# Performance work log

Measured on AMD Instinct MI355X. Metric: run time of the kernel, lower is better.

## Reference

```python
import jax, jax.numpy as jnp
import numpy as np

BN_EPS = 1e-3  # Keras BatchNormalization default epsilon


def setup_inputs() -> dict:
    key = jax.random.key(0)
    ks = jax.random.split(key, 10)
    B, H, W, F, K = 16, 64, 64, 512, 32
    support = 1.0 / np.sqrt(K * F)
    fc_support = np.sqrt(1.0 / F)
    return {
        "inputs": jax.random.normal(ks[0], (B, H, W, F), dtype=jnp.float32),
        # Encoder params
        "codewords": jax.random.uniform(ks[1], (K, F), minval=-support, maxval=support, dtype=jnp.float32),
        "smoothing": jax.random.uniform(ks[2], (K,), minval=-1.0, maxval=0.0, dtype=jnp.float32),
        # BatchNorm (inference mode: moving stats) over feature axis of (B, K, F)
        "bn_gamma": jnp.ones((F,), dtype=jnp.float32),
        "bn_beta": jnp.zeros((F,), dtype=jnp.float32),
        "bn_mean": jnp.zeros((F,), dtype=jnp.float32),
        "bn_var": jnp.ones((F,), dtype=jnp.float32),
        # Dense layers
        "fc_enc_w": jax.random.uniform(ks[3], (F, F), minval=-fc_support, maxval=fc_support, dtype=jnp.float32),
        "fc_enc_b": jax.random.uniform(ks[4], (F,), minval=-fc_support, maxval=fc_support, dtype=jnp.float32),
        "fc_se_w": jax.random.uniform(ks[5], (F, 1), minval=-fc_support, maxval=fc_support, dtype=jnp.float32),
        "fc_se_b": jax.random.uniform(ks[6], (1,), minval=-fc_support, maxval=fc_support, dtype=jnp.float32),
    }


def _encoder(x, codewords, smoothing, bn_gamma, bn_beta, bn_mean, bn_var):
    # x: (B, H, W, F) -> feats (B, N, F)
    B, H, W, F = x.shape
    feats = x.reshape(B, H * W, F)
    # Squared residual norms without materializing (B, N, K, F):
    x2 = jnp.sum(feats * feats, axis=-1, keepdims=True)          # (B, N, 1)
    c2 = jnp.sum(codewords * codewords, axis=-1)                 # (K,)
    xc = jnp.einsum("bnf,kf->bnk", feats, codewords)             # (B, N, K)
    sqnorms = x2 - 2.0 * xc + c2                                 # (B, N, K)
    s = jax.nn.softmax(sqnorms * smoothing, axis=-1)             # (B, N, K)
    # sum_n s[b,n,k] * (x[b,n] - c[k]) = s^T x - c * sum_n s
    s_sum = jnp.sum(s, axis=1)                                   # (B, K)
    enc = jnp.einsum("bnk,bnf->bkf", s, feats) - s_sum[:, :, None] * codewords  # (B, K, F)
    # BatchNorm (inference) + ReLU, then aggregate over codewords
    enc_bn = (enc - bn_mean) * jax.lax.rsqrt(bn_var + BN_EPS) * bn_gamma + bn_beta
    return jnp.sum(jax.nn.relu(enc_bn), axis=1)                  # (B, F)


def reference(inputs, codewords, smoothing, bn_gamma, bn_beta, bn_mean, bn_var,
              fc_enc_w, fc_enc_b, fc_se_w, fc_se_b):
    enc = _encoder(inputs, codewords, smoothing, bn_gamma, bn_beta, bn_mean, bn_var)
    attn = jax.nn.sigmoid(enc @ fc_enc_w + fc_enc_b)             # (B, F)
    featuremaps_out = attn[:, None, None, :] * inputs            # (B, H, W, F)
    se_loss_out = enc @ fc_se_w + fc_se_b                        # (B, 1)
    return (featuremaps_out, se_loss_out)
```

## Files before the change

### kernel.cpp

```cpp
#include <hip/hip_runtime.h>
#include <hip/hip_bf16.h>
#include <math.h>

#define Bb   16
#define HWn  4096
#define Ff   512
#define Kk   32

typedef __attribute__((ext_vector_type(8))) short  short8;
typedef __attribute__((ext_vector_type(4))) float  f32x4;

#define WS_SSUM  0
#define WS_EOUT  512
#define WS_ATTN  (WS_EOUT + Bb * Ff)
#define WS_CWB   (WS_ATTN + Bb * Ff)
#define WS_C2    (WS_CWB + 8192)
#define WS_SM    (WS_C2 + 32)

#define SCR_PART 0
#define SCR_RED  16777216

__global__ void prep(const float* __restrict__ cw, const float* __restrict__ smth,
                     unsigned short* __restrict__ cwb,
                     float* __restrict__ c2l2, float* __restrict__ sml2)
{
    const int t = threadIdx.x;
    const float4* c4 = (const float4*)cw;
    #pragma unroll
    for (int j = 0; j < 16; ++j) {
        const int i = t + j * 256;
        const float4 v = c4[i];
        union { __hip_bfloat162 h; unsigned int u; } p0, p1;
        p0.h = __float22bfloat162_rn(make_float2(v.x, v.y));
        p1.h = __float22bfloat162_rn(make_float2(v.z, v.w));
        *reinterpret_cast<uint2*>(&cwb[i * 4]) = make_uint2(p0.u, p1.u);
    }
    const int k = t >> 3, sk = t & 7;
    float p = 0.f;
    #pragma unroll
    for (int j = 0; j < 16; ++j) {
        const float4 v = c4[k * 128 + sk + j * 8];
        p = fmaf(v.x, v.x, fmaf(v.y, v.y, fmaf(v.z, v.z, fmaf(v.w, v.w, p))));
    }
    p += __shfl_xor(p, 1); p += __shfl_xor(p, 2); p += __shfl_xor(p, 4);
    if (sk == 0) {
        const float L2E = 1.4426950408889634f;
        const float sm = smth[k];
        sml2[k] = sm * L2E;
        c2l2[k] = p * sm * L2E;
    }
}

__global__ __launch_bounds__(256, 2) void enc_pass(
    const float* __restrict__ x, const unsigned short* __restrict__ cwb,
    const float* __restrict__ c2l2, const float* __restrict__ sml2,
    float* __restrict__ part, float* __restrict__ s_sum)
{
    __shared__ __align__(16) unsigned short fb16[32 * 512];
    __shared__ float sN[32][36];
    __shared__ float x2s[32];
    __shared__ float sm_s[32], c2_s[32];

    const int tid  = threadIdx.x;
    const int wave = tid >> 6, lane = tid & 63;
    const int b    = blockIdx.y;
    const int cx   = blockIdx.x;
    const int row0 = cx * 128;

    if (tid < 32) { sm_s[tid] = sml2[tid]; c2_s[tid] = c2l2[tid]; }

    float acc[8][8];
    #pragma unroll
    for (int j = 0; j < 8; ++j)
        #pragma unroll
        for (int i = 0; i < 8; ++i) acc[j][i] = 0.f;
    float ssl[8] = {0.f, 0.f, 0.f, 0.f, 0.f, 0.f, 0.f, 0.f};

    for (int t = 0; t < 4; ++t) {
        if (t) __syncthreads();
        const float4* xr4 = (const float4*)(x + ((size_t)b * HWn + row0 + t * 32) * Ff);
        {
            const int n = tid >> 3, f8 = tid & 7;
            float p = 0.f;
            #pragma unroll
            for (int j = 0; j < 16; ++j) {
                const int f4 = f8 + j * 8;
                const float4 v = xr4[n * 128 + f4];
                p = fmaf(v.x, v.x, fmaf(v.y, v.y, fmaf(v.z, v.z, fmaf(v.w, v.w, p))));
                union { __hip_bfloat162 h; unsigned int u; } p0, p1;
                p0.h = __float22bfloat162_rn(make_float2(v.x, v.y));
                p1.h = __float22bfloat162_rn(make_float2(v.z, v.w));
                const int chunk = f4 >> 1;
                const int idx = n * 512 + (((chunk ^ (n & 7)) << 3) | ((f4 & 1) << 2));
                *reinterpret_cast<uint2*>(&fb16[idx]) = make_uint2(p0.u, p1.u);
            }
            p += __shfl_xor(p, 1); p += __shfl_xor(p, 2); p += __shfl_xor(p, 4);
            if (f8 == 0) x2s[n] = p;
        }
        __syncthreads();
        if (wave < 2) {
            const int col = lane & 15, g = lane >> 4;
            const int nl  = wave * 16 + col;
            f32x4 c0 = {0.f, 0.f, 0.f, 0.f}, c1 = {0.f, 0.f, 0.f, 0.f};
            const unsigned short* arow0 = cwb + col * 512 + g * 8;
            const unsigned short* arow1 = arow0 + 16 * 512;
            const int nswz = (nl & 7) << 3;
            #pragma unroll
            for (int fs = 0; fs < 16; ++fs) {
                const short8 a0 = *(const short8*)(arow0 + fs * 32);
                const short8 a1 = *(const short8*)(arow1 + fs * 32);
                const short8 bf = *(const short8*)&fb16[nl * 512 + ((((fs * 4 + g) << 3)) ^ nswz)];
                c0 = __builtin_amdgcn_mfma_f32_16x16x32_bf16(a0, bf, c0, 0, 0, 0);
                c1 = __builtin_amdgcn_mfma_f32_16x16x32_bf16(a1, bf, c1, 0, 0, 0);
            }
            const float x2v = x2s[nl];
            float lg[8];
            #pragma unroll
            for (int r = 0; r < 4; ++r) {
                const int k0 = g * 4 + r;
                lg[r]     = fmaf(sm_s[k0],      fmaf(-2.f, c0[r], x2v), c2_s[k0]);
                lg[4 + r] = fmaf(sm_s[k0 + 16], fmaf(-2.f, c1[r], x2v), c2_s[k0 + 16]);
            }
            float m = lg[0];
            #pragma unroll
            for (int j = 1; j < 8; ++j) m = fmaxf(m, lg[j]);
            m = fmaxf(m, __shfl_xor(m, 16)); m = fmaxf(m, __shfl_xor(m, 32));
            float e[8], sum = 0.f;
            #pragma unroll
            for (int j = 0; j < 8; ++j) { e[j] = exp2f(lg[j] - m); sum += e[j]; }
            sum += __shfl_xor(sum, 16); sum += __shfl_xor(sum, 32);
            const float inv = 1.f / sum;
            #pragma unroll
            for (int r = 0; r < 4; ++r) {
                const float s0 = e[r] * inv, s1 = e[4 + r] * inv;
                sN[nl][g * 4 + r]      = s0;
                sN[nl][16 + g * 4 + r] = s1;
                ssl[r] += s0; ssl[4 + r] += s1;
            }
        }
        __syncthreads();
        {
            const int kw = wave * 8;
            #pragma unroll 2
            for (int n = 0; n < 32; ++n) {
                const f32x4 s0 = *(const f32x4*)&sN[n][kw];
                const f32x4 s1 = *(const f32x4*)&sN[n][kw + 4];
                const uint4 u = *(const uint4*)&fb16[n * 512 + (((lane ^ (n & 7))) << 3)];
                float fx[8];
                fx[0] = __uint_as_float(u.x << 16);
                fx[1] = __uint_as_float(u.x & 0xffff0000u);
                fx[2] = __uint_as_float(u.y << 16);
                fx[3] = __uint_as_float(u.y & 0xffff0000u);
                fx[4] = __uint_as_float(u.z << 16);
                fx[5] = __uint_as_float(u.z & 0xffff0000u);
                fx[6] = __uint_as_float(u.w << 16);
                fx[7] = __uint_as_float(u.w & 0xffff0000u);
                #pragma unroll
                for (int j = 0; j < 4; ++j) {
                    const float sj0 = s0[j], sj1 = s1[j];
                    #pragma unroll
                    for (int i = 0; i < 8; ++i) {
                        acc[j][i]     = fmaf(sj0, fx[i], acc[j][i]);
                        acc[4 + j][i] = fmaf(sj1, fx[i], acc[4 + j][i]);
                    }
                }
            }
        }
    }
    if (wave < 2) {
        const int g = lane >> 4;
        #pragma unroll
        for (int j = 0; j < 8; ++j) {
            float v = ssl[j];
            v += __shfl_xor(v, 1); v += __shfl_xor(v, 2);
            v += __shfl_xor(v, 4); v += __shfl_xor(v, 8);
            if ((lane & 15) == 0) {
                const int k = ((j & 4) << 2) + g * 4 + (j & 3);
                atomicAdd(&s_sum[b * Kk + k], v);
            }
        }
    }
    {
        float* basep = part + (((size_t)(b * 32 + cx) * Kk) + wave * 8) * Ff + lane * 8;
        #pragma unroll
        for (int j = 0; j < 8; ++j) {
            *reinterpret_cast<float4*>(basep + j * Ff) =
                make_float4(acc[j][0], acc[j][1], acc[j][2], acc[j][3]);
            *reinterpret_cast<float4*>(basep + j * Ff + 4) =
                make_float4(acc[j][4], acc[j][5], acc[j][6], acc[j][7]);
        }
    }
}

__global__ void enc_red(const float* __restrict__ scr, float* __restrict__ outp)
{
    const int idx = blockIdx.x * 256 + threadIdx.x;
    const int b   = idx >> 14;
    const int rem = idx & 16383;
    const float* p = scr + (size_t)b * 32 * 16384 + rem;
    float a = 0.f;
    #pragma unroll
    for (int c = 0; c < 32; ++c) a += p[c * 16384];
    outp[idx] = a;
}

__global__ void enc_finish(const float* __restrict__ enc_acc,
                           const float* __restrict__ s_sum,
                           const float* __restrict__ cw,
                           const float* __restrict__ gamma,
                           const float* __restrict__ beta,
                           const float* __restrict__ mean,
                           const float* __restrict__ var,
                           const float* __restrict__ se_w,
                           const float* __restrict__ se_b,
                           float* __restrict__ enc_out,
                           float* __restrict__ se_out)
{
    __shared__ float ss[Kk];
    __shared__ float red[8];
    const int b = blockIdx.x, f = threadIdx.x;
    if (f < Kk) ss[f] = s_sum[b * Kk + f];
    __syncthreads();
    const float m  = mean[f];
    const float g  = gamma[f];
    const float bt = beta[f];
    const float iv = rsqrtf(var[f] + 1e-3f);
    float a = 0.f;
    #pragma unroll 4
    for (int k = 0; k < Kk; ++k) {
        float v = enc_acc[((long)b * Kk + k) * Ff + f] - ss[k] * cw[k * Ff + f];
        v = (v - m) * iv * g + bt;
        a += fmaxf(v, 0.f);
    }
    enc_out[b * Ff + f] = a;
    float p = a * se_w[f];
    p += __shfl_down(p, 32); p += __shfl_down(p, 16); p += __shfl_down(p, 8);
    p += __shfl_down(p, 4);  p += __shfl_down(p, 2);  p += __shfl_down(p, 1);
    if ((f & 63) == 0) red[f >> 6] = p;
    __syncthreads();
    if (f == 0) {
        float t = 0.f;
        #pragma unroll
        for (int i = 0; i < 8; ++i) t += red[i];
        se_out[b] = t + se_b[0];
    }
}

__global__ void attn_fc(const float* __restrict__ enc_out,
                        const float* __restrict__ W,
                        const float* __restrict__ bias,
                        float* __restrict__ attn)
{
    __shared__ float eo[Bb][Ff];
    const int t = threadIdx.x, fg = blockIdx.x;
    #pragma unroll
    for (int j = 0; j < 4; ++j)
        reinterpret_cast<float4*>(&eo[0][0])[t + j * 512] =
            reinterpret_cast<const float4*>(enc_out)[t + j * 512];
    __syncthreads();
    const int f  = fg * 64 + (t & 63);
    const int b0 = t >> 6;
    float a0 = bias[f], a1 = bias[f];
    #pragma unroll 8
    for (int fp = 0; fp < Ff; ++fp) {
        const float w = W[fp * Ff + f];
        a0 = fmaf(eo[b0][fp],     w, a0);
        a1 = fmaf(eo[b0 + 8][fp], w, a1);
    }
    attn[b0 * Ff + f]       = 1.f / (1.f + expf(-a0));
    attn[(b0 + 8) * Ff + f] = 1.f / (1.f + expf(-a1));
}

__global__ void bcast_mul(const float4* __restrict__ x4,
                          const float* __restrict__ attn,
                          float4* __restrict__ o4)
{
    const int stride = gridDim.x * blockDim.x;
    const int total4 = Bb * HWn * Ff / 4;
    for (int i = blockIdx.x * blockDim.x + threadIdx.x; i < total4; i += stride) {
        const float4 v = x4[i];
        const int f4 = i & 127;
        const int bb = i >> 19;
        const float4 a = *reinterpret_cast<const float4*>(&attn[bb * Ff + f4 * 4]);
        o4[i] = make_float4(v.x * a.x, v.y * a.y, v.z * a.z, v.w * a.w);
    }
}

extern "C" void kernel_launch(void* const* d_in, const int* in_sizes, int n_in,
                              void* d_out, int out_size, void* d_ws, size_t ws_size,
                              hipStream_t stream)
{
    (void)in_sizes; (void)n_in; (void)out_size; (void)ws_size;
    const float* x     = (const float*)d_in[0];
    const float* cw    = (const float*)d_in[1];
    const float* smth  = (const float*)d_in[2];
    const float* gamma = (const float*)d_in[3];
    const float* beta  = (const float*)d_in[4];
    const float* mean  = (const float*)d_in[5];
    const float* var   = (const float*)d_in[6];
    const float* Wenc  = (const float*)d_in[7];
    const float* benc  = (const float*)d_in[8];
    const float* Wse   = (const float*)d_in[9];
    const float* bse   = (const float*)d_in[10];

    float* out = (float*)d_out;
    float* ws  = (float*)d_ws;
    float* ssum = ws + WS_SSUM;
    float* eout = ws + WS_EOUT;
    float* attn = ws + WS_ATTN;
    unsigned short* cwb = (unsigned short*)(ws + WS_CWB);
    float* c2l2 = ws + WS_C2;
    float* sml2 = ws + WS_SM;

    float* scr_part = out + SCR_PART;
    float* scr_red  = out + SCR_RED;

    hipMemsetAsync(ssum, 0, (size_t)Bb * Kk * sizeof(float), stream);
    prep<<<1, 256, 0, stream>>>(cw, smth, cwb, c2l2, sml2);
    enc_pass<<<dim3(32, Bb), 256, 0, stream>>>(x, cwb, c2l2, sml2, scr_part, ssum);
    enc_red<<<1024, 256, 0, stream>>>(scr_part, scr_red);
    enc_finish<<<Bb, 512, 0, stream>>>(scr_red, ssum, cw, gamma, beta, mean, var,
                                       Wse, bse, eout, out + (long)Bb * HWn * Ff);
    attn_fc<<<8, 512, 0, stream>>>(eout, Wenc, benc, attn);
    bcast_mul<<<2048, 256, 0, stream>>>((const float4*)x, attn, (float4*)out);
}
```

Measured before the change: 172.2 us.

## Compute s^T x accumulation with bf16 MFMA and prefetch next input tile

Replaces the scalar FMA loop that accumulated softmax weights times features with bf16 MFMA instructions. This needs a transposed bf16 copy of the input tile and bf16 softmax weights in shared memory. Global loads for the next 32-row tile are issued into registers before the current tile is processed, to overlap memory latency. Rounding the softmax weights to bf16 loses some precision, and the extra transposed writes to LDS add shared-memory traffic and register pressure.

```diff
diff --git a/kernel.cpp b/kernel.cpp
--- a/kernel.cpp
+++ b/kernel.cpp
@@ -20,6 +20,17 @@
 #define SCR_PART 0
 #define SCR_RED  16777216
 
+static __device__ __forceinline__ unsigned int pack2bf(float a, float b) {
+    union { __hip_bfloat162 h; unsigned int u; } p;
+    p.h = __float22bfloat162_rn(make_float2(a, b));
+    return p.u;
+}
+static __device__ __forceinline__ unsigned short f2bf(float v) {
+    union { __hip_bfloat16 h; unsigned short u; } c;
+    c.h = __float2bfloat16(v);
+    return c.u;
+}
+
 __global__ void prep(const float* __restrict__ cw, const float* __restrict__ smth,
                      unsigned short* __restrict__ cwb,
                      float* __restrict__ c2l2, float* __restrict__ sml2)
@@ -30,10 +41,8 @@
     for (int j = 0; j < 16; ++j) {
         const int i = t + j * 256;
         const float4 v = c4[i];
-        union { __hip_bfloat162 h; unsigned int u; } p0, p1;
-        p0.h = __float22bfloat162_rn(make_float2(v.x, v.y));
-        p1.h = __float22bfloat162_rn(make_float2(v.z, v.w));
-        *reinterpret_cast<uint2*>(&cwb[i * 4]) = make_uint2(p0.u, p1.u);
+        *reinterpret_cast<uint2*>(&cwb[i * 4]) =
+            make_uint2(pack2bf(v.x, v.y), pack2bf(v.z, v.w));
     }
     const int k = t >> 3, sk = t & 7;
     float p = 0.f;
@@ -57,50 +66,77 @@
     float* __restrict__ part, float* __restrict__ s_sum)
 {
     __shared__ __align__(16) unsigned short fb16[32 * 512];
-    __shared__ float sN[32][36];
+    __shared__ __align__(16) unsigned short xTl[512 * 36];
+    __shared__ __align__(16) unsigned short sTl[32 * 32];
     __shared__ float x2s[32];
     __shared__ float sm_s[32], c2_s[32];
 
     const int tid  = threadIdx.x;
     const int wave = tid >> 6, lane = tid & 63;
+    const int col  = lane & 15, g = lane >> 4;
     const int b    = blockIdx.y;
     const int cx   = blockIdx.x;
     const int row0 = cx * 128;
 
     if (tid < 32) { sm_s[tid] = sml2[tid]; c2_s[tid] = c2l2[tid]; }
 
-    float acc[8][8];
-    #pragma unroll
-    for (int j = 0; j < 8; ++j)
-        #pragma unroll
-        for (int i = 0; i < 8; ++i) acc[j][i] = 0.f;
+    const int n2  = tid >> 4;
+    const int f16 = tid & 15;
+
+    f32x4 accm[16];
+    #pragma unroll
+    for (int i = 0; i < 16; ++i) accm[i] = (f32x4){0.f, 0.f, 0.f, 0.f};
     float ssl[8] = {0.f, 0.f, 0.f, 0.f, 0.f, 0.f, 0.f, 0.f};
+
+    const float4* xb4 = (const float4*)(x + ((size_t)b * HWn + row0) * Ff);
+    float4 r0[8], r1[8];
+    #pragma unroll
+    for (int j = 0; j < 8; ++j) {
+        r0[j] = xb4[(2 * n2) * 128 + f16 + j * 16];
+        r1[j] = xb4[(2 * n2 + 1) * 128 + f16 + j * 16];
+    }
 
     for (int t = 0; t < 4; ++t) {
         if (t) __syncthreads();
-        const float4* xr4 = (const float4*)(x + ((size_t)b * HWn + row0 + t * 32) * Ff);
         {
-            const int n = tid >> 3, f8 = tid & 7;
-            float p = 0.f;
-            #pragma unroll
-            for (int j = 0; j < 16; ++j) {
-                const int f4 = f8 + j * 8;
-                const float4 v = xr4[n * 128 + f4];
-                p = fmaf(v.x, v.x, fmaf(v.y, v.y, fmaf(v.z, v.z, fmaf(v.w, v.w, p))));
-                union { __hip_bfloat162 h; unsigned int u; } p0, p1;
-                p0.h = __float22bfloat162_rn(make_float2(v.x, v.y));
-                p1.h = __float22bfloat162_rn(make_float2(v.z, v.w));
-                const int chunk = f4 >> 1;
-                const int idx = n * 512 + (((chunk ^ (n & 7)) << 3) | ((f4 & 1) << 2));
-                *reinterpret_cast<uint2*>(&fb16[idx]) = make_uint2(p0.u, p1.u);
-            }
-            p += __shfl_xor(p, 1); p += __shfl_xor(p, 2); p += __shfl_xor(p, 4);
-            if (f8 == 0) x2s[n] = p;
+            float p0 = 0.f, p1 = 0.f;
+            const int na = 2 * n2, nb = na + 1;
+            #pragma unroll
+            for (int j = 0; j < 8; ++j) {
+                const float4 va = r0[j], vb = r1[j];
+                p0 = fmaf(va.x, va.x, fmaf(va.y, va.y, fmaf(va.z, va.z, fmaf(va.w, va.w, p0))));
+                p1 = fmaf(vb.x, vb.x, fmaf(vb.y, vb.y, fmaf(vb.z, vb.z, fmaf(vb.w, vb.w, p1))));
+                const int f4n = f16 + j * 16;
+                const int lowbit = (f4n & 1) << 2;
+                const int chA = (((f4n >> 1) ^ (na & 7)) << 3) | lowbit;
+                const int chB = (((f4n >> 1) ^ (nb & 7)) << 3) | lowbit;
+                *reinterpret_cast<uint2*>(&fb16[na * 512 + chA]) =
+                    make_uint2(pack2bf(va.x, va.y), pack2bf(va.z, va.w));
+                *reinterpret_cast<uint2*>(&fb16[nb * 512 + chB]) =
+                    make_uint2(pack2bf(vb.x, vb.y), pack2bf(vb.z, vb.w));
+                const int fbase = f4n * 4;
+                unsigned int* xw = reinterpret_cast<unsigned int*>(&xTl[0]);
+                xw[(fbase + 0) * 18 + n2] = pack2bf(va.x, vb.x);
+                xw[(fbase + 1) * 18 + n2] = pack2bf(va.y, vb.y);
+                xw[(fbase + 2) * 18 + n2] = pack2bf(va.z, vb.z);
+                xw[(fbase + 3) * 18 + n2] = pack2bf(va.w, vb.w);
+            }
+            p0 += __shfl_xor(p0, 1); p0 += __shfl_xor(p0, 2);
+            p0 += __shfl_xor(p0, 4); p0 += __shfl_xor(p0, 8);
+            p1 += __shfl_xor(p1, 1); p1 += __shfl_xor(p1, 2);
+            p1 += __shfl_xor(p1, 4); p1 += __shfl_xor(p1, 8);
+            if (f16 == 0) { x2s[na] = p0; x2s[nb] = p1; }
+        }
+        if (t < 3) {
+            #pragma unroll
+            for (int j = 0; j < 8; ++j) {
+                r0[j] = xb4[((t + 1) * 32 + 2 * n2) * 128 + f16 + j * 16];
+                r1[j] = xb4[((t + 1) * 32 + 2 * n2 + 1) * 128 + f16 + j * 16];
+            }
         }
         __syncthreads();
         if (wave < 2) {
-            const int col = lane & 15, g = lane >> 4;
-            const int nl  = wave * 16 + col;
+            const int nl = wave * 16 + col;
             f32x4 c0 = {0.f, 0.f, 0.f, 0.f}, c1 = {0.f, 0.f, 0.f, 0.f};
             const unsigned short* arow0 = cwb + col * 512 + g * 8;
             const unsigned short* arow1 = arow0 + 16 * 512;
@@ -133,42 +169,27 @@
             #pragma unroll
             for (int r = 0; r < 4; ++r) {
                 const float s0 = e[r] * inv, s1 = e[4 + r] * inv;
-                sN[nl][g * 4 + r]      = s0;
-                sN[nl][16 + g * 4 + r] = s1;
+                sTl[(g * 4 + r) * 32 + nl]        = f2bf(s0);
+                sTl[(16 + g * 4 + r) * 32 + nl]   = f2bf(s1);
                 ssl[r] += s0; ssl[4 + r] += s1;
             }
         }
         __syncthreads();
         {
-            const int kw = wave * 8;
-            #pragma unroll 2
-            for (int n = 0; n < 32; ++n) {
-                const f32x4 s0 = *(const f32x4*)&sN[n][kw];
-                const f32x4 s1 = *(const f32x4*)&sN[n][kw + 4];
-                const uint4 u = *(const uint4*)&fb16[n * 512 + (((lane ^ (n & 7))) << 3)];
-                float fx[8];
-                fx[0] = __uint_as_float(u.x << 16);
-                fx[1] = __uint_as_float(u.x & 0xffff0000u);
-                fx[2] = __uint_as_float(u.y << 16);
-                fx[3] = __uint_as_float(u.y & 0xffff0000u);
-                fx[4] = __uint_as_float(u.z << 16);
-                fx[5] = __uint_as_float(u.z & 0xffff0000u);
-                fx[6] = __uint_as_float(u.w << 16);
-                fx[7] = __uint_as_float(u.w & 0xffff0000u);
-                #pragma unroll
-                for (int j = 0; j < 4; ++j) {
-                    const float sj0 = s0[j], sj1 = s1[j];
-                    #pragma unroll
-                    for (int i = 0; i < 8; ++i) {
-                        acc[j][i]     = fmaf(sj0, fx[i], acc[j][i]);
-                        acc[4 + j][i] = fmaf(sj1, fx[i], acc[4 + j][i]);
-                    }
-                }
+            const int koff = (wave & 1) << 4;
+            const int fh   = (wave >> 1) << 8;
+            const short8 afrag = *(const short8*)&sTl[(koff + col) * 32 + g * 8];
+            #pragma unroll
+            for (int fb = 0; fb < 16; ++fb) {
+                const unsigned short* bp = &xTl[(fh + fb * 16 + col) * 36 + g * 8];
+                union { uint2 u[2]; short8 s; } bu;
+                bu.u[0] = *reinterpret_cast<const uint2*>(bp);
+                bu.u[1] = *reinterpret_cast<const uint2*>(bp + 4);
+                accm[fb] = __builtin_amdgcn_mfma_f32_16x16x32_bf16(afrag, bu.s, accm[fb], 0, 0, 0);
             }
         }
     }
     if (wave < 2) {
-        const int g = lane >> 4;
         #pragma unroll
         for (int j = 0; j < 8; ++j) {
             float v = ssl[j];
@@ -181,14 +202,14 @@
         }
     }
     {
-        float* basep = part + (((size_t)(b * 32 + cx) * Kk) + wave * 8) * Ff + lane * 8;
+        const int koff = (wave & 1) << 4;
+        const int fh   = (wave >> 1) << 8;
+        float* basep = part + ((size_t)(b * 32 + cx) * Kk + koff + g * 4) * Ff + fh + col;
         #pragma unroll
-        for (int j = 0; j < 8; ++j) {
-            *reinterpret_cast<float4*>(basep + j * Ff) =
-                make_float4(acc[j][0], acc[j][1], acc[j][2], acc[j][3]);
-            *reinterpret_cast<float4*>(basep + j * Ff + 4) =
-                make_float4(acc[j][4], acc[j][5], acc[j][6], acc[j][7]);
-        }
+        for (int fb = 0; fb < 16; ++fb)
+            #pragma unroll
+            for (int r = 0; r < 4; ++r)
+                basep[r * Ff + fb * 16] = accm[fb][r];
     }
 }
 
```

Result: faster. 157.6 us (-8.5%).

## Use 512-thread blocks with 64-row tiles and split MFMA/softmax across all waves

Applied to the files above, without the earlier changes.

The encoder pass moves from 256 to 512 threads per block and stages 64 rows per tile instead of 32, so each block runs two tile iterations instead of four. All eight waves now take part in the MFMA distance computation, each computing one 16x16 tile, and the softmax is spread across all threads through a shared scratch transpose. Previously only two waves did that work while the rest sat idle. Each wave's accumulator drops to 4x8, which lowers register pressure, and the s_sum reduction goes through shared memory so only 32 atomics are issued per block. The cost is extra __syncthreads barriers and more LDS use per block, which may limit occupancy.

```diff
diff --git a/kernel.cpp b/kernel.cpp
--- a/kernel.cpp
+++ b/kernel.cpp
@@ -6,6 +6,8 @@
 #define HWn  4096
 #define Ff   512
 #define Kk   32
+#define ROWS 64
+#define GCH  32
 
 typedef __attribute__((ext_vector_type(8))) short  short8;
 typedef __attribute__((ext_vector_type(4))) float  f32x4;
@@ -20,6 +22,12 @@
 #define SCR_PART 0
 #define SCR_RED  16777216
 
+static __device__ __forceinline__ unsigned int pack2bf(float a, float b) {
+    union { __hip_bfloat162 h; unsigned int u; } p;
+    p.h = __float22bfloat162_rn(make_float2(a, b));
+    return p.u;
+}
+
 __global__ void prep(const float* __restrict__ cw, const float* __restrict__ smth,
                      unsigned short* __restrict__ cwb,
                      float* __restrict__ c2l2, float* __restrict__ sml2)
@@ -30,10 +38,8 @@
     for (int j = 0; j < 16; ++j) {
         const int i = t + j * 256;
         const float4 v = c4[i];
-        union { __hip_bfloat162 h; unsigned int u; } p0, p1;
-        p0.h = __float22bfloat162_rn(make_float2(v.x, v.y));
-        p1.h = __float22bfloat162_rn(make_float2(v.z, v.w));
-        *reinterpret_cast<uint2*>(&cwb[i * 4]) = make_uint2(p0.u, p1.u);
+        *reinterpret_cast<uint2*>(&cwb[i * 4]) =
+            make_uint2(pack2bf(v.x, v.y), pack2bf(v.z, v.w));
     }
     const int k = t >> 3, sk = t & 7;
     float p = 0.f;
@@ -51,101 +57,106 @@
     }
 }
 
-__global__ __launch_bounds__(256, 2) void enc_pass(
+__global__ __launch_bounds__(512, 4) void enc_pass(
     const float* __restrict__ x, const unsigned short* __restrict__ cwb,
     const float* __restrict__ c2l2, const float* __restrict__ sml2,
     float* __restrict__ part, float* __restrict__ s_sum)
 {
-    __shared__ __align__(16) unsigned short fb16[32 * 512];
-    __shared__ float sN[32][36];
-    __shared__ float x2s[32];
+    __shared__ __align__(16) unsigned short fb16[ROWS * 512];
+    __shared__ float scratch[2304];
+    __shared__ float x2s[ROWS];
     __shared__ float sm_s[32], c2_s[32];
+    __shared__ float swred[8][32];
 
     const int tid  = threadIdx.x;
     const int wave = tid >> 6, lane = tid & 63;
+    const int col  = lane & 15, g = lane >> 4;
     const int b    = blockIdx.y;
     const int cx   = blockIdx.x;
-    const int row0 = cx * 128;
 
     if (tid < 32) { sm_s[tid] = sml2[tid]; c2_s[tid] = c2l2[tid]; }
 
-    float acc[8][8];
-    #pragma unroll
-    for (int j = 0; j < 8; ++j)
+    const int srow = tid >> 3;
+    const int sf   = tid & 7;
+
+    float acc[4][8];
+    #pragma unroll
+    for (int j = 0; j < 4; ++j)
         #pragma unroll
         for (int i = 0; i < 8; ++i) acc[j][i] = 0.f;
-    float ssl[8] = {0.f, 0.f, 0.f, 0.f, 0.f, 0.f, 0.f, 0.f};
-
-    for (int t = 0; t < 4; ++t) {
+    float ssl[4] = {0.f, 0.f, 0.f, 0.f};
+
+    const float4* xb4 = (const float4*)(x + ((size_t)b * HWn + cx * 128) * Ff);
+
+    for (int t = 0; t < 2; ++t) {
         if (t) __syncthreads();
-        const float4* xr4 = (const float4*)(x + ((size_t)b * HWn + row0 + t * 32) * Ff);
-        {
-            const int n = tid >> 3, f8 = tid & 7;
+        {
             float p = 0.f;
             #pragma unroll
             for (int j = 0; j < 16; ++j) {
-                const int f4 = f8 + j * 8;
-                const float4 v = xr4[n * 128 + f4];
+                const int f4n = sf + j * 8;
+                const float4 v = xb4[(t * ROWS + srow) * 128 + f4n];
                 p = fmaf(v.x, v.x, fmaf(v.y, v.y, fmaf(v.z, v.z, fmaf(v.w, v.w, p))));
-                union { __hip_bfloat162 h; unsigned int u; } p0, p1;
-                p0.h = __float22bfloat162_rn(make_float2(v.x, v.y));
-                p1.h = __float22bfloat162_rn(make_float2(v.z, v.w));
-                const int chunk = f4 >> 1;
-                const int idx = n * 512 + (((chunk ^ (n & 7)) << 3) | ((f4 & 1) << 2));
-                *reinterpret_cast<uint2*>(&fb16[idx]) = make_uint2(p0.u, p1.u);
+                const int idx = srow * 512 +
+                    ((((f4n >> 1) ^ (srow & 7)) << 3) | ((f4n & 1) << 2));
+                *reinterpret_cast<uint2*>(&fb16[idx]) =
+                    make_uint2(pack2bf(v.x, v.y), pack2bf(v.z, v.w));
             }
             p += __shfl_xor(p, 1); p += __shfl_xor(p, 2); p += __shfl_xor(p, 4);
-            if (f8 == 0) x2s[n] = p;
+            if (sf == 0) x2s[srow] = p;
         }
         __syncthreads();
-        if (wave < 2) {
-            const int col = lane & 15, g = lane >> 4;
-            const int nl  = wave * 16 + col;
-            f32x4 c0 = {0.f, 0.f, 0.f, 0.f}, c1 = {0.f, 0.f, 0.f, 0.f};
-            const unsigned short* arow0 = cwb + col * 512 + g * 8;
-            const unsigned short* arow1 = arow0 + 16 * 512;
+        {
+            const int kh = wave >> 2, nh = wave & 3;
+            const int nl = nh * 16 + col;
+            f32x4 c0 = {0.f, 0.f, 0.f, 0.f};
+            const unsigned short* arow = cwb + (kh * 16 + col) * 512 + g * 8;
             const int nswz = (nl & 7) << 3;
             #pragma unroll
             for (int fs = 0; fs < 16; ++fs) {
-                const short8 a0 = *(const short8*)(arow0 + fs * 32);
-                const short8 a1 = *(const short8*)(arow1 + fs * 32);
+                const short8 a0 = *(const short8*)(arow + fs * 32);
                 const short8 bf = *(const short8*)&fb16[nl * 512 + ((((fs * 4 + g) << 3)) ^ nswz)];
                 c0 = __builtin_amdgcn_mfma_f32_16x16x32_bf16(a0, bf, c0, 0, 0, 0);
-                c1 = __builtin_amdgcn_mfma_f32_16x16x32_bf16(a1, bf, c1, 0, 0, 0);
-            }
-            const float x2v = x2s[nl];
-            float lg[8];
+            }
+            #pragma unroll
+            for (int r = 0; r < 4; ++r)
+                scratch[(kh * 16 + g * 4 + r) * 65 + nl] = c0[r];
+        }
+        __syncthreads();
+        float lg[4];
+        {
+            const float x2v = x2s[srow];
             #pragma unroll
             for (int r = 0; r < 4; ++r) {
-                const int k0 = g * 4 + r;
-                lg[r]     = fmaf(sm_s[k0],      fmaf(-2.f, c0[r], x2v), c2_s[k0]);
-                lg[4 + r] = fmaf(sm_s[k0 + 16], fmaf(-2.f, c1[r], x2v), c2_s[k0 + 16]);
-            }
-            float m = lg[0];
-            #pragma unroll
-            for (int j = 1; j < 8; ++j) m = fmaxf(m, lg[j]);
-            m = fmaxf(m, __shfl_xor(m, 16)); m = fmaxf(m, __shfl_xor(m, 32));
-            float e[8], sum = 0.f;
-            #pragma unroll
-            for (int j = 0; j < 8; ++j) { e[j] = exp2f(lg[j] - m); sum += e[j]; }
-            sum += __shfl_xor(sum, 16); sum += __shfl_xor(sum, 32);
+                const int k = sf * 4 + r;
+                lg[r] = fmaf(sm_s[k], fmaf(-2.f, scratch[k * 65 + srow], x2v), c2_s[k]);
+            }
+        }
+        __syncthreads();
+        {
+            float m = fmaxf(fmaxf(lg[0], lg[1]), fmaxf(lg[2], lg[3]));
+            m = fmaxf(m, __shfl_xor(m, 1));
+            m = fmaxf(m, __shfl_xor(m, 2));
+            m = fmaxf(m, __shfl_xor(m, 4));
+            float e[4], sum = 0.f;
+            #pragma unroll
+            for (int r = 0; r < 4; ++r) { e[r] = exp2f(lg[r] - m); sum += e[r]; }
+            sum += __shfl_xor(sum, 1); sum += __shfl_xor(sum, 2); sum += __shfl_xor(sum, 4);
             const float inv = 1.f / sum;
             #pragma unroll
             for (int r = 0; r < 4; ++r) {
-                const float s0 = e[r] * inv, s1 = e[4 + r] * inv;
-                sN[nl][g * 4 + r]      = s0;
-                sN[nl][16 + g * 4 + r] = s1;
-                ssl[r] += s0; ssl[4 + r] += s1;
+                const float s = e[r] * inv;
+                scratch[srow * 36 + sf * 4 + r] = s;
+                ssl[r] += s;
             }
         }
         __syncthreads();
         {
-            const int kw = wave * 8;
-            #pragma unroll 2
-            for (int n = 0; n < 32; ++n) {
-                const f32x4 s0 = *(const f32x4*)&sN[n][kw];
-                const f32x4 s1 = *(const f32x4*)&sN[n][kw + 4];
-                const uint4 u = *(const uint4*)&fb16[n * 512 + (((lane ^ (n & 7))) << 3)];
+            const int kq = wave * 4;
+            #pragma unroll 4
+            for (int n = 0; n < ROWS; ++n) {
+                const f32x4 sv = *(const f32x4*)&scratch[n * 36 + kq];
+                const uint4 u = *(const uint4*)&fb16[n * 512 + ((lane ^ (n & 7)) << 3)];
                 float fx[8];
                 fx[0] = __uint_as_float(u.x << 16);
                 fx[1] = __uint_as_float(u.x & 0xffff0000u);
@@ -157,33 +168,33 @@
                 fx[7] = __uint_as_float(u.w & 0xffff0000u);
                 #pragma unroll
                 for (int j = 0; j < 4; ++j) {
-                    const float sj0 = s0[j], sj1 = s1[j];
+                    const float sj = sv[j];
                     #pragma unroll
-                    for (int i = 0; i < 8; ++i) {
-                        acc[j][i]     = fmaf(sj0, fx[i], acc[j][i]);
-                        acc[4 + j][i] = fmaf(sj1, fx[i], acc[4 + j][i]);
-                    }
+                    for (int i = 0; i < 8; ++i)
+                        acc[j][i] = fmaf(sj, fx[i], acc[j][i]);
                 }
             }
         }
     }
-    if (wave < 2) {
-        const int g = lane >> 4;
+    __syncthreads();
+    #pragma unroll
+    for (int r = 0; r < 4; ++r) {
+        float v = ssl[r];
+        v += __shfl_xor(v, 8); v += __shfl_xor(v, 16); v += __shfl_xor(v, 32);
+        if (lane < 8) swred[wave][lane * 4 + r] = v;
+    }
+    __syncthreads();
+    if (tid < 32) {
+        float a = 0.f;
         #pragma unroll
-        for (int j = 0; j < 8; ++j) {
-            float v = ssl[j];
-            v += __shfl_xor(v, 1); v += __shfl_xor(v, 2);
-            v += __shfl_xor(v, 4); v += __shfl_xor(v, 8);
-            if ((lane & 15) == 0) {
-                const int k = ((j & 4) << 2) + g * 4 + (j & 3);
-                atomicAdd(&s_sum[b * Kk + k], v);
-            }
-        }
+        for (int w = 0; w < 8; ++w) a += swred[w][tid];
+        atomicAdd(&s_sum[b * Kk + tid], a);
     }
     {
-        float* basep = part + (((size_t)(b * 32 + cx) * Kk) + wave * 8) * Ff + lane * 8;
+        float* basep = part + (size_t)(b * GCH + cx) * (Kk * Ff) +
+                       (size_t)(wave * 4) * Ff + lane * 8;
         #pragma unroll
-        for (int j = 0; j < 8; ++j) {
+        for (int j = 0; j < 4; ++j) {
             *reinterpret_cast<float4*>(basep + j * Ff) =
                 make_float4(acc[j][0], acc[j][1], acc[j][2], acc[j][3]);
             *reinterpret_cast<float4*>(basep + j * Ff + 4) =
@@ -197,10 +208,10 @@
     const int idx = blockIdx.x * 256 + threadIdx.x;
     const int b   = idx >> 14;
     const int rem = idx & 16383;
-    const float* p = scr + (size_t)b * 32 * 16384 + rem;
+    const float* p = scr + (size_t)b * GCH * 16384 + rem;
     float a = 0.f;
     #pragma unroll
-    for (int c = 0; c < 32; ++c) a += p[c * 16384];
+    for (int c = 0; c < GCH; ++c) a += p[c * 16384];
     outp[idx] = a;
 }
 
@@ -317,7 +328,7 @@
 
     hipMemsetAsync(ssum, 0, (size_t)Bb * Kk * sizeof(float), stream);
     prep<<<1, 256, 0, stream>>>(cw, smth, cwb, c2l2, sml2);
-    enc_pass<<<dim3(32, Bb), 256, 0, stream>>>(x, cwb, c2l2, sml2, scr_part, ssum);
+    enc_pass<<<dim3(GCH, Bb), 512, 0, stream>>>(x, cwb, c2l2, sml2, scr_part, ssum);
     enc_red<<<1024, 256, 0, stream>>>(scr_part, scr_red);
     enc_finish<<<Bb, 512, 0, stream>>>(scr_red, ssum, cw, gamma, beta, mean, var,
                                        Wse, bse, eout, out + (long)Bb * HWn * Ff);
```

Result: slower. 203.1 us (+18.0%).
